# Performance work log

Measured on AMD Instinct MI355X. Metric: run time of the kernel, lower is better.

The kernel has to match this reference:

```python
import jax, jax.numpy as jnp
import numpy as np

SIGMA = 0.2
BN_EPS = 1e-5


def setup_inputs() -> dict:
    key = jax.random.key(0)
    k1, k2, k3, k4 = jax.random.split(key, 4)
    B, F, K, M = 8, 16384, 3, 64
    normals = jax.random.normal(k1, (B, 3, F), dtype=jnp.float32)
    # normalize to unit vectors (face normals), keeps math well-conditioned
    normals = normals / jnp.linalg.norm(normals, axis=1, keepdims=True)
    weight_alpha = jax.random.uniform(k2, (1, M, 4), dtype=jnp.float32) * np.pi
    weight_beta = jax.random.uniform(k3, (1, M, 4), dtype=jnp.float32) * 2 * np.pi
    bn_gamma = jnp.ones((M,), dtype=jnp.float32)
    bn_beta = jnp.zeros((M,), dtype=jnp.float32)
    neighbor_index = jax.random.randint(k4, (B, F, K), 0, F, dtype=jnp.int64)
    return {"normals": normals, "weight_alpha": weight_alpha,
            "weight_beta": weight_beta, "bn_gamma": bn_gamma,
            "bn_beta": bn_beta, "neighbor_index": neighbor_index}


def reference(normals, weight_alpha, weight_beta, bn_gamma, bn_beta, neighbor_index):
    # normals: [B, 3, F]; neighbor_index: [B, F, K]
    B, _, F = normals.shape
    K = neighbor_index.shape[-1]
    # kernel points on unit sphere from spherical angles: [3, M, 4]
    sa, ca = jnp.sin(weight_alpha), jnp.cos(weight_alpha)
    sb, cb = jnp.sin(weight_beta), jnp.cos(weight_beta)
    w = jnp.concatenate([sa * cb, sa * sb, ca], axis=0)  # [3, M, 4]

    nt = jnp.transpose(normals, (0, 2, 1))  # [B, F, 3]
    # gather neighbor normals per batch: [B, F, K, 3]
    neigh = jax.vmap(lambda n, idx: n[idx])(nt, neighbor_index)
    # points per face: center + K neighbors -> [B, F, K+1, 3]
    pts = jnp.concatenate([nt[:, :, None, :], neigh], axis=2)

    # squared distance via expansion: ||p||^2 + ||w||^2 - 2 p.w
    dot = jnp.einsum('bfic,cmj->bmfij', pts, w)        # [B, M, F, K+1, 4]
    p2 = jnp.sum(pts * pts, axis=-1)                   # [B, F, K+1]
    w2 = jnp.sum(w * w, axis=0)                        # [M, 4]
    dist = (p2[:, None, :, :, None] + w2[None, :, None, None, :] - 2.0 * dot)

    feat = jnp.sum(jnp.exp(dist / (-2.0 * SIGMA ** 2)), axis=(3, 4))
    feat = feat / float((K + 1) * 4)                   # [B, M, F]

    # BatchNorm1d (training-mode batch stats over B and F per channel M)
    mean = jnp.mean(feat, axis=(0, 2), keepdims=True)
    var = jnp.var(feat, axis=(0, 2), keepdims=True)
    xhat = (feat - mean) / jnp.sqrt(var + BN_EPS)
    out = xhat * bn_gamma[None, :, None] + bn_beta[None, :, None]
    return jax.nn.relu(out)
```

## Files before the change

kernel.cpp:

```cpp
#include <hip/hip_runtime.h>

#define B_DIM 8
#define F_DIM 16384
#define K_DIM 3
#define M_DIM 64
#define MCH   16
#define LOG2E 1.4426950408889634f

#define WS_S 0
#define WS_Q 512
#define WS_A 1024
#define WS_C 1088

__global__ __launch_bounds__(256) void fkc_feat_kernel(
    const float* __restrict__ normals,
    const float* __restrict__ walpha,
    const float* __restrict__ wbeta,
    const int*   __restrict__ nidx,
    float* __restrict__ feat_out)
{
    __shared__ float4 sW[MCH * 4];
    const int tid = threadIdx.x;
    const int b  = blockIdx.x >> 8;
    const int mc = (blockIdx.x >> 6) & 3;
    const int fc = blockIdx.x & 63;

    if (tid < MCH * 4) {
        int idx = mc * MCH * 4 + tid;
        float a = walpha[idx], bb = wbeta[idx];
        float sa = sinf(a), ca = cosf(a);
        float sb = sinf(bb), cb = cosf(bb);
        float wx = sa * cb, wy = sa * sb, wz = ca;
        float w2 = wx * wx + wy * wy + wz * wz;
        sW[tid] = make_float4(wx * 25.0f * LOG2E, wy * 25.0f * LOG2E,
                              wz * 25.0f * LOG2E, -12.5f * LOG2E * (w2 + 1.0f));
    }
    __syncthreads();

    const int f = (fc << 8) + tid;
    const float* nb = normals + (size_t)b * 3 * F_DIM;
    float px[4], py[4], pz[4];
    px[0] = nb[f]; py[0] = nb[F_DIM + f]; pz[0] = nb[2 * F_DIM + f];
    const int* ib = nidx + ((size_t)b * F_DIM + f) * K_DIM;
#pragma unroll
    for (int k = 0; k < K_DIM; ++k) {
        int id = ib[k];
        px[k + 1] = nb[id]; py[k + 1] = nb[F_DIM + id]; pz[k + 1] = nb[2 * F_DIM + id];
    }

    float* outb = feat_out + ((size_t)b * M_DIM + mc * MCH) * F_DIM + f;
#pragma unroll 2
    for (int m = 0; m < MCH; ++m) {
        float s0 = 0.f, s1 = 0.f, s2 = 0.f, s3 = 0.f;
#pragma unroll
        for (int j = 0; j < 4; ++j) {
            float4 w = sW[m * 4 + j];
            s0 += __builtin_amdgcn_exp2f(fmaf(w.x, px[0], fmaf(w.y, py[0], fmaf(w.z, pz[0], w.w))));
            s1 += __builtin_amdgcn_exp2f(fmaf(w.x, px[1], fmaf(w.y, py[1], fmaf(w.z, pz[1], w.w))));
            s2 += __builtin_amdgcn_exp2f(fmaf(w.x, px[2], fmaf(w.y, py[2], fmaf(w.z, pz[2], w.w))));
            s3 += __builtin_amdgcn_exp2f(fmaf(w.x, px[3], fmaf(w.y, py[3], fmaf(w.z, pz[3], w.w))));
        }
        outb[(size_t)m * F_DIM] = ((s0 + s1) + (s2 + s3)) * (1.0f / 16.0f);
    }
}

__global__ __launch_bounds__(256) void fkc_sum_kernel(const float* __restrict__ feat,
                                                      float* __restrict__ ws)
{
    __shared__ float sS[4], sQ[4];
    const int row = blockIdx.x;
    const int b = row >> 6, m = row & 63;
    const int tid = threadIdx.x;
    const float4* p4 = (const float4*)(feat + (size_t)row * F_DIM);

    float s = 0.f, q = 0.f;
#pragma unroll
    for (int i = 0; i < 16; ++i) {
        float4 v = p4[tid + i * 256];
        s += (v.x + v.y) + (v.z + v.w);
        q += (v.x * v.x + v.y * v.y) + (v.z * v.z + v.w * v.w);
    }
#pragma unroll
    for (int off = 32; off >= 1; off >>= 1) {
        s += __shfl_xor(s, off, 64);
        q += __shfl_xor(q, off, 64);
    }
    const int wave = tid >> 6, lane = tid & 63;
    if (lane == 0) { sS[wave] = s; sQ[wave] = q; }
    __syncthreads();
    if (tid == 0) {
        ws[WS_S + m * 8 + b] = (sS[0] + sS[1]) + (sS[2] + sS[3]);
        ws[WS_Q + m * 8 + b] = (sQ[0] + sQ[1]) + (sQ[2] + sQ[3]);
    }
}

__global__ void fkc_stats_kernel(const float* __restrict__ gamma,
                                 const float* __restrict__ beta,
                                 float* __restrict__ ws)
{
    int m = threadIdx.x;
    if (m < M_DIM) {
        float s = 0.f, q = 0.f;
#pragma unroll
        for (int b = 0; b < B_DIM; ++b) {
            s += ws[WS_S + m * 8 + b];
            q += ws[WS_Q + m * 8 + b];
        }
        const float invcnt = 1.0f / (float)(B_DIM * F_DIM);
        float mean = s * invcnt;
        float var  = q * invcnt - mean * mean;
        float inv  = rsqrtf(var + 1e-5f);
        float A = gamma[m] * inv;
        ws[WS_A + m] = A;
        ws[WS_C + m] = beta[m] - mean * A;
    }
}

__global__ __launch_bounds__(256) void fkc_bn_kernel(float* __restrict__ out,
                                                     const float* __restrict__ ws)
{
    size_t i4 = (size_t)blockIdx.x * blockDim.x + threadIdx.x;
    int m = (int)((i4 >> 12) & 63);
    float A = ws[WS_A + m];
    float C = ws[WS_C + m];
    float4 v = reinterpret_cast<float4*>(out)[i4];
    v.x = fmaxf(fmaf(v.x, A, C), 0.0f);
    v.y = fmaxf(fmaf(v.y, A, C), 0.0f);
    v.z = fmaxf(fmaf(v.z, A, C), 0.0f);
    v.w = fmaxf(fmaf(v.w, A, C), 0.0f);
    reinterpret_cast<float4*>(out)[i4] = v;
}

extern "C" void kernel_launch(void* const* d_in, const int* in_sizes, int n_in,
                              void* d_out, int out_size, void* d_ws, size_t ws_size,
                              hipStream_t stream)
{
    const float* normals = (const float*)d_in[0];
    const float* walpha  = (const float*)d_in[1];
    const float* wbeta   = (const float*)d_in[2];
    const float* gamma   = (const float*)d_in[3];
    const float* beta    = (const float*)d_in[4];
    const int*   nidx    = (const int*)d_in[5];
    float* out = (float*)d_out;
    float* ws  = (float*)d_ws;

    hipLaunchKernelGGL(fkc_feat_kernel, dim3(2048), dim3(256), 0, stream,
                       normals, walpha, wbeta, nidx, out);
    hipLaunchKernelGGL(fkc_sum_kernel, dim3(B_DIM * M_DIM), dim3(256), 0, stream,
                       out, ws);
    hipLaunchKernelGGL(fkc_stats_kernel, dim3(1), dim3(64), 0, stream,
                       gamma, beta, ws);
    hipLaunchKernelGGL(fkc_bn_kernel, dim3(8192), dim3(256), 0, stream,
                       out, ws);
}
```

Measured before the change: 55.94 us.

## Fuse per-channel sum/sumsq into feature kernel and fold stats into BN pass

The feature kernel now computes per-block partial sums and sums of squares for each channel, using shuffles and shared memory, and writes them to the workspace. This removes the separate pass that re-read the whole 32 MB feature tensor. The stats and BN kernels are merged: each row block reduces the 512 partials for its channel, computes the scale and shift, and applies BN+ReLU in place. This cuts two launches and one full read of the tensor, at the cost of some redundant per-block stat reduction and extra shuffle and LDS work in the compute kernel.

```diff
diff --git a/kernel.cpp b/kernel.cpp
--- a/kernel.cpp
+++ b/kernel.cpp
@@ -7,19 +7,20 @@
 #define MCH   16
 #define LOG2E 1.4426950408889634f
 
-#define WS_S 0
-#define WS_Q 512
-#define WS_A 1024
-#define WS_C 1088
+#define WS_Q 32768
 
 __global__ __launch_bounds__(256) void fkc_feat_kernel(
     const float* __restrict__ normals,
     const float* __restrict__ walpha,
     const float* __restrict__ wbeta,
     const int*   __restrict__ nidx,
-    float* __restrict__ feat_out)
+    float* __restrict__ feat_out,
+    float* __restrict__ ws)
 {
     __shared__ float4 sW[MCH * 4];
+    __shared__ float sRS[MCH][32];
+    __shared__ float sRQ[MCH][32];
+
     const int tid = threadIdx.x;
     const int b  = blockIdx.x >> 8;
     const int mc = (blockIdx.x >> 6) & 3;
@@ -48,6 +49,7 @@
         px[k + 1] = nb[id]; py[k + 1] = nb[F_DIM + id]; pz[k + 1] = nb[2 * F_DIM + id];
     }
 
+    const int wave = tid >> 6, lane = tid & 63;
     float* outb = feat_out + ((size_t)b * M_DIM + mc * MCH) * F_DIM + f;
 #pragma unroll 2
     for (int m = 0; m < MCH; ++m) {
@@ -60,75 +62,81 @@
             s2 += __builtin_amdgcn_exp2f(fmaf(w.x, px[2], fmaf(w.y, py[2], fmaf(w.z, pz[2], w.w))));
             s3 += __builtin_amdgcn_exp2f(fmaf(w.x, px[3], fmaf(w.y, py[3], fmaf(w.z, pz[3], w.w))));
         }
-        outb[(size_t)m * F_DIM] = ((s0 + s1) + (s2 + s3)) * (1.0f / 16.0f);
+        float fv = ((s0 + s1) + (s2 + s3)) * (1.0f / 16.0f);
+        outb[(size_t)m * F_DIM] = fv;
+
+        float s = fv, q = fv * fv;
+        s += __shfl_xor(s, 8, 64);  q += __shfl_xor(q, 8, 64);
+        s += __shfl_xor(s, 16, 64); q += __shfl_xor(q, 16, 64);
+        s += __shfl_xor(s, 32, 64); q += __shfl_xor(q, 32, 64);
+        if (lane < 8) { sRS[m][wave * 8 + lane] = s; sRQ[m][wave * 8 + lane] = q; }
+    }
+    __syncthreads();
+
+    {
+        const int m = tid >> 4, j = tid & 15;
+        float s = sRS[m][j] + sRS[m][j + 16];
+        float q = sRQ[m][j] + sRQ[m][j + 16];
+        s += __shfl_xor(s, 1, 64);  q += __shfl_xor(q, 1, 64);
+        s += __shfl_xor(s, 2, 64);  q += __shfl_xor(q, 2, 64);
+        s += __shfl_xor(s, 4, 64);  q += __shfl_xor(q, 4, 64);
+        s += __shfl_xor(s, 8, 64);  q += __shfl_xor(q, 8, 64);
+        if (j == 0) {
+            int slot = (mc * MCH + m) * 512 + b * 64 + fc;
+            ws[slot] = s;
+            ws[WS_Q + slot] = q;
+        }
     }
 }
 
-__global__ __launch_bounds__(256) void fkc_sum_kernel(const float* __restrict__ feat,
-                                                      float* __restrict__ ws)
+__global__ __launch_bounds__(256) void fkc_bn_kernel(
+    float* __restrict__ out,
+    const float* __restrict__ gamma,
+    const float* __restrict__ beta,
+    const float* __restrict__ ws)
 {
     __shared__ float sS[4], sQ[4];
+    __shared__ float sAC[2];
     const int row = blockIdx.x;
-    const int b = row >> 6, m = row & 63;
+    const int m = row & 63;
     const int tid = threadIdx.x;
-    const float4* p4 = (const float4*)(feat + (size_t)row * F_DIM);
+    const int wave = tid >> 6, lane = tid & 63;
 
-    float s = 0.f, q = 0.f;
+    {
+        float s = ws[m * 512 + tid]         + ws[m * 512 + tid + 256];
+        float q = ws[WS_Q + m * 512 + tid]  + ws[WS_Q + m * 512 + tid + 256];
 #pragma unroll
-    for (int i = 0; i < 16; ++i) {
-        float4 v = p4[tid + i * 256];
-        s += (v.x + v.y) + (v.z + v.w);
-        q += (v.x * v.x + v.y * v.y) + (v.z * v.z + v.w * v.w);
+        for (int off = 32; off >= 1; off >>= 1) {
+            s += __shfl_xor(s, off, 64);
+            q += __shfl_xor(q, off, 64);
+        }
+        if (lane == 0) { sS[wave] = s; sQ[wave] = q; }
     }
-#pragma unroll
-    for (int off = 32; off >= 1; off >>= 1) {
-        s += __shfl_xor(s, off, 64);
-        q += __shfl_xor(q, off, 64);
-    }
-    const int wave = tid >> 6, lane = tid & 63;
-    if (lane == 0) { sS[wave] = s; sQ[wave] = q; }
     __syncthreads();
     if (tid == 0) {
-        ws[WS_S + m * 8 + b] = (sS[0] + sS[1]) + (sS[2] + sS[3]);
-        ws[WS_Q + m * 8 + b] = (sQ[0] + sQ[1]) + (sQ[2] + sQ[3]);
-    }
-}
-
-__global__ void fkc_stats_kernel(const float* __restrict__ gamma,
-                                 const float* __restrict__ beta,
-                                 float* __restrict__ ws)
-{
-    int m = threadIdx.x;
-    if (m < M_DIM) {
-        float s = 0.f, q = 0.f;
-#pragma unroll
-        for (int b = 0; b < B_DIM; ++b) {
-            s += ws[WS_S + m * 8 + b];
-            q += ws[WS_Q + m * 8 + b];
-        }
+        float s = (sS[0] + sS[1]) + (sS[2] + sS[3]);
+        float q = (sQ[0] + sQ[1]) + (sQ[2] + sQ[3]);
         const float invcnt = 1.0f / (float)(B_DIM * F_DIM);
         float mean = s * invcnt;
         float var  = q * invcnt - mean * mean;
         float inv  = rsqrtf(var + 1e-5f);
         float A = gamma[m] * inv;
-        ws[WS_A + m] = A;
-        ws[WS_C + m] = beta[m] - mean * A;
+        sAC[0] = A;
+        sAC[1] = beta[m] - mean * A;
     }
-}
+    __syncthreads();
 
-__global__ __launch_bounds__(256) void fkc_bn_kernel(float* __restrict__ out,
-                                                     const float* __restrict__ ws)
-{
-    size_t i4 = (size_t)blockIdx.x * blockDim.x + threadIdx.x;
-    int m = (int)((i4 >> 12) & 63);
-    float A = ws[WS_A + m];
-    float C = ws[WS_C + m];
-    float4 v = reinterpret_cast<float4*>(out)[i4];
-    v.x = fmaxf(fmaf(v.x, A, C), 0.0f);
-    v.y = fmaxf(fmaf(v.y, A, C), 0.0f);
-    v.z = fmaxf(fmaf(v.z, A, C), 0.0f);
-    v.w = fmaxf(fmaf(v.w, A, C), 0.0f);
-    reinterpret_cast<float4*>(out)[i4] = v;
+    const float A = sAC[0], C = sAC[1];
+    float4* p4 = (float4*)(out + (size_t)row * F_DIM);
+#pragma unroll
+    for (int i = 0; i < 16; ++i) {
+        float4 v = p4[tid + i * 256];
+        v.x = fmaxf(fmaf(v.x, A, C), 0.0f);
+        v.y = fmaxf(fmaf(v.y, A, C), 0.0f);
+        v.z = fmaxf(fmaf(v.z, A, C), 0.0f);
+        v.w = fmaxf(fmaf(v.w, A, C), 0.0f);
+        p4[tid + i * 256] = v;
+    }
 }
 
 extern "C" void kernel_launch(void* const* d_in, const int* in_sizes, int n_in,
@@ -145,11 +153,7 @@
     float* ws  = (float*)d_ws;
 
     hipLaunchKernelGGL(fkc_feat_kernel, dim3(2048), dim3(256), 0, stream,
-                       normals, walpha, wbeta, nidx, out);
-    hipLaunchKernelGGL(fkc_sum_kernel, dim3(B_DIM * M_DIM), dim3(256), 0, stream,
-                       out, ws);
-    hipLaunchKernelGGL(fkc_stats_kernel, dim3(1), dim3(64), 0, stream,
-                       gamma, beta, ws);
-    hipLaunchKernelGGL(fkc_bn_kernel, dim3(8192), dim3(256), 0, stream,
-                       out, ws);
+                       normals, walpha, wbeta, nidx, out, ws);
+    hipLaunchKernelGGL(fkc_bn_kernel, dim3(B_DIM * M_DIM), dim3(256), 0, stream,
+                       out, gamma, beta, ws);
 }
```

After: 50.85 us. 9.1% less time.
